# Performance work log

Measured on AMD Instinct MI355X. Metric: run time of the kernel, lower is better.

The kernel has to match this reference:

```python
import jax, jax.numpy as jnp
import numpy as np

N_HEAD = 16
HEAD_DIM = 64
N_EMBD = N_HEAD * HEAD_DIM  # 1024


def setup_inputs() -> dict:
    key = jax.random.key(0)
    ks = jax.random.split(key, 5)
    B, S = 2, 2048
    x = jax.random.normal(ks[0], (B, S, N_EMBD), dtype=jnp.float32)
    qkv_w = jax.random.normal(ks[1], (N_EMBD, 3 * N_EMBD), dtype=jnp.float32) * 0.02
    qkv_b = jax.random.normal(ks[2], (3 * N_EMBD,), dtype=jnp.float32) * 0.02
    proj_w = jax.random.normal(ks[3], (N_EMBD, N_EMBD), dtype=jnp.float32) * 0.02
    proj_b = jax.random.normal(ks[4], (N_EMBD,), dtype=jnp.float32) * 0.02
    return {"x": x, "qkv_w": qkv_w, "qkv_b": qkv_b, "proj_w": proj_w, "proj_b": proj_b}


def reference(x, qkv_w, qkv_b, proj_w, proj_b):
    B, S, _ = x.shape
    qkv = x @ qkv_w + qkv_b  # [B,S,3E]
    q, k, v = jnp.split(qkv, 3, axis=-1)
    # [B,H,S,D]
    q = q.reshape(B, S, N_HEAD, HEAD_DIM).transpose(0, 2, 1, 3)
    k = k.reshape(B, S, N_HEAD, HEAD_DIM).transpose(0, 2, 1, 3)
    v = v.reshape(B, S, N_HEAD, HEAD_DIM).transpose(0, 2, 1, 3)
    scale = 1.0 / jnp.sqrt(jnp.float32(HEAD_DIM))
    scores = jnp.einsum('bhqd,bhkd->bhqk', q, k) * scale  # [B,H,S,S]
    causal = jnp.tril(jnp.ones((S, S), dtype=bool))
    scores = jnp.where(causal[None, None], scores, jnp.float32(-jnp.inf))
    attn = jax.nn.softmax(scores, axis=-1)  # dropout p=0 (eval)
    out = jnp.einsum('bhqk,bhkd->bhqd', attn, v)
    out = out.transpose(0, 2, 1, 3).reshape(B, S, N_EMBD)
    out = out @ proj_w + proj_b  # resid dropout p=0
    return out, k, v
```

## Files before the change

### kernel.cpp

```cpp
#include <hip/hip_runtime.h>
#include <hip/hip_bf16.h>


typedef __attribute__((ext_vector_type(4))) float f32x4;
typedef __attribute__((ext_vector_type(16))) float f32x16;
typedef __attribute__((ext_vector_type(8))) short s16x8;
typedef __attribute__((ext_vector_type(4))) short s16x4;

__device__ __forceinline__ short f2bf(float f) {
    union { float f; unsigned u; } x{f};
    unsigned r = x.u + 0x7fff + ((x.u >> 16) & 1);
    return (short)(r >> 16);
}

__device__ __forceinline__ void gload_lds16(const void* g, void* l) {
    __builtin_amdgcn_global_load_lds(
        (const __attribute__((address_space(1))) void*)g,
        (__attribute__((address_space(3))) void*)l, 16, 0, 0);
}

__global__ __launch_bounds__(256) void fused_prepass(const float* __restrict__ x,
                                                     short* __restrict__ x_bf,
                                                     const float* __restrict__ qkv_w,
                                                     short* __restrict__ wT1,
                                                     const float* __restrict__ proj_w,
                                                     short* __restrict__ wT2) {
    __shared__ float tile[32][33];
    const int bid = blockIdx.x, tid = threadIdx.x;
    if (bid < 2048) {
        int i = (bid * 256 + tid) * 8;
        f32x4 a = *(const f32x4*)&x[i];
        f32x4 b = *(const f32x4*)&x[i + 4];
        s16x8 o;
        #pragma unroll
        for (int j = 0; j < 4; ++j) o[j] = f2bf(a[j]);
        #pragma unroll
        for (int j = 0; j < 4; ++j) o[j + 4] = f2bf(b[j]);
        *(s16x8*)&x_bf[i] = o;
        return;
    }
    const float* in;
    short* out;
    int K = 1024, N, n0, k0;
    if (bid < 5120) {
        int blk = bid - 2048;
        in = qkv_w; out = wT1; N = 3072;
        n0 = (blk % 96) * 32; k0 = (blk / 96) * 32;
    } else {
        int blk = bid - 5120;
        in = proj_w; out = wT2; N = 1024;
        n0 = (blk & 31) * 32; k0 = (blk >> 5) * 32;
    }
    const int tx = tid & 31, ty = tid >> 5;
    #pragma unroll
    for (int r = 0; r < 4; ++r)
        tile[ty + r * 8][tx] = in[(long)(k0 + ty + r * 8) * N + n0 + tx];
    __syncthreads();
    #pragma unroll
    for (int r = 0; r < 4; ++r)
        out[(long)(n0 + ty + r * 8) * K + k0 + tx] = f2bf(tile[tx][ty + r * 8]);
}

template <int MODE>
__global__ __launch_bounds__(256) void gemm_bf16(
    const short* __restrict__ A, const short* __restrict__ Bt,
    const float* __restrict__ bias, int M, int N, int K,
    float* __restrict__ outf,
    short* __restrict__ qbf, short* __restrict__ kbf, short* __restrict__ vbfT,
    float* __restrict__ kout, float* __restrict__ vout) {
    __shared__ __align__(16) short As[128 * 64];
    __shared__ __align__(16) short Bs[128 * 64];
    const int tid = threadIdx.x;
    const int l = tid & 63, w = tid >> 6;
    const int lr = l >> 4, lc = l & 15;
    const int wm = w >> 1, wn = w & 1;
    const int bid = blockIdx.x;
    const int xcd = bid & 7, s = bid >> 3;
    int bx, by;
    if (MODE == 1) { bx = (xcd & 1) * 12 + s % 12; by = (xcd >> 1) * 8 + s / 12; }
    else           { bx = (xcd & 1) * 4 + (s & 3); by = (xcd >> 1) * 8 + (s >> 2); }
    const int m0 = by * 128, n0 = bx * 128;

    f32x4 acc[4][4] = {};

    for (int kb = 0; kb < K; kb += 64) {
        __syncthreads();
        #pragma unroll
        for (int j = 0; j < 4; ++j) {
            const int c = tid + 256 * j;
            const int row = c >> 3;
            const int lseg = (c & 7) ^ (row & 7);
            gload_lds16(A + (long)(m0 + row) * K + kb + lseg * 8, As + c * 8);
            gload_lds16(Bt + (long)(n0 + row) * K + kb + lseg * 8, Bs + c * 8);
        }
        __syncthreads();
        #pragma unroll
        for (int kh = 0; kh < 2; ++kh) {
            s16x8 af[4], bfr[4];
            #pragma unroll
            for (int mi = 0; mi < 4; ++mi) {
                const int row = wm * 64 + mi * 16 + lc;
                af[mi] = *(const s16x8*)&As[row * 64 + (((kh * 4 + lr) ^ (lc & 7)) * 8)];
            }
            #pragma unroll
            for (int ni = 0; ni < 4; ++ni) {
                const int row = wn * 64 + ni * 16 + lc;
                bfr[ni] = *(const s16x8*)&Bs[row * 64 + (((kh * 4 + lr) ^ (lc & 7)) * 8)];
            }
            #pragma unroll
            for (int mi = 0; mi < 4; ++mi)
                #pragma unroll
                for (int ni = 0; ni < 4; ++ni)
                    acc[mi][ni] = __builtin_amdgcn_mfma_f32_16x16x32_bf16(
                        af[mi], bfr[ni], acc[mi][ni], 0, 0, 0);
        }
    }

    #pragma unroll
    for (int mi = 0; mi < 4; ++mi) {
        #pragma unroll
        for (int ni = 0; ni < 4; ++ni) {
            int col = n0 + wn * 64 + ni * 16 + lc;
            float bv = bias[col];
            if (MODE == 1) {
                int sec = col >> 10, rem = col & 1023;
                int h = rem >> 6, d = rem & 63;
                int row0 = m0 + wm * 64 + mi * 16 + lr * 4;
                int b = row0 >> 11, s0 = row0 & 2047;
                long idxSD = ((long)((b << 4) + h) * 2048 + s0) * 64 + d;
                if (sec == 0) {
                    #pragma unroll
                    for (int i = 0; i < 4; ++i) {
                        float val = acc[mi][ni][i] + bv;
                        qbf[idxSD + (long)i * 64] = f2bf(val * 0.1803368801111244f);
                    }
                } else if (sec == 1) {
                    #pragma unroll
                    for (int i = 0; i < 4; ++i) {
                        float val = acc[mi][ni][i] + bv;
                        kout[idxSD + (long)i * 64] = val;
                        kbf[idxSD + (long)i * 64] = f2bf(val);
                    }
                } else {
                    s16x4 pk;
                    #pragma unroll
                    for (int i = 0; i < 4; ++i) {
                        float val = acc[mi][ni][i] + bv;
                        vout[idxSD + (long)i * 64] = val;
                        pk[i] = f2bf(val);
                    }
                    *(s16x4*)&vbfT[((long)((b << 4) + h) * 64 + d) * 2048 + s0] = pk;
                }
            } else {
                #pragma unroll
                for (int i = 0; i < 4; ++i) {
                    int row = m0 + wm * 64 + mi * 16 + lr * 4 + i;
                    outf[(long)row * N + col] = acc[mi][ni][i] + bv;
                }
            }
        }
    }
}

__global__ __launch_bounds__(512, 4) void attn_kernel(const short* __restrict__ qbf,
                                                      const short* __restrict__ kbf,
                                                      const short* __restrict__ vbfT,
                                                      short* __restrict__ obf) {
    const int bid = blockIdx.x;
    const int xcd = bid & 7, r = bid >> 3;
    const int head_local = r & 3, q16 = r >> 2;
    const int qt = (q16 < 8) ? (q16 + 8) : (15 - q16);
    const int bh = xcd * 4 + head_local;
    const int tid = threadIdx.x;
    const int wv = tid >> 6, l = tid & 63;
    const int strip = wv & 3, kh = wv >> 2;
    const int h = l >> 5;
    const int l8 = l & 7;
    const int q0 = qt * 128 + strip * 32;
    const int qlane = q0 + (l & 31);
    const long baseSD = (long)bh * 2048 * 64;
    const long baseDS = (long)bh * 64 * 2048;

    __shared__ __align__(16) short Ks[2][64 * 64];
    __shared__ __align__(16) short Vs[2][64 * 64];
    __shared__ __align__(16) float MG[4][64][36];

    const int sSub = l >> 3;
    const int sChunk = (l & 7) ^ sSub;
    auto stage = [&](int kt, int nb) {
        const int k0 = kt * 64;
        const int r0 = wv * 8 + sSub;
        gload_lds16(kbf + baseSD + (long)(k0 + r0) * 64 + sChunk * 8,
                    &Ks[nb][(wv * 8) * 64]);
        gload_lds16(vbfT + baseDS + (long)r0 * 2048 + k0 + sChunk * 8,
                    &Vs[nb][(wv * 8) * 64]);
    };

    s16x8 qf[4];
    #pragma unroll
    for (int dd = 0; dd < 4; ++dd)
        qf[dd] = *(const s16x8*)&qbf[baseSD + (long)qlane * 64 + dd * 16 + h * 8];

    f32x4 lacc = {};
    f32x16 O[2] = {};

    const int nkt = 2 * qt + 2;

    stage(0, 0);
    __syncthreads();
    int cur = 0;

    for (int kt = 0; kt < nkt; ++kt) {
        if (kt + 1 < nkt) stage(kt + 1, cur ^ 1);
        const int kbase = kt * 64 + kh * 32;

        if (kbase <= q0 + 31) {
            const short* Kb = Ks[cur];
            const short* Vb = Vs[cur];
            f32x16 z = {};
            #pragma unroll
            for (int dd = 0; dd < 4; ++dd) {
                s16x8 kf = *(const s16x8*)&Kb[(kh * 32 + (l & 31)) * 64 +
                                              (((2 * dd + h) ^ l8) * 8)];
                z = __builtin_amdgcn_mfma_f32_32x32x16_bf16(kf, qf[dd], z, 0, 0, 0);
            }
            if (kbase + 31 > q0) {
                #pragma unroll
                for (int rr = 0; rr < 16; ++rr) {
                    int kpos = kbase + (rr & 3) + 8 * (rr >> 2) + 4 * h;
                    if (kpos > qlane) z[rr] = -INFINITY;
                }
            }
            float p[16];
            #pragma unroll
            for (int rr = 0; rr < 16; ++rr) {
                p[rr] = __builtin_amdgcn_exp2f(z[rr]);
                lacc[rr & 3] += p[rr];
            }
            #pragma unroll
            for (int f = 0; f < 2; ++f) {
                union { __hip_bfloat162 b2[4]; s16x8 v; } pk;
                #pragma unroll
                for (int j = 0; j < 4; ++j)
                    pk.b2[j] = __float22bfloat162_rn(
                        make_float2(p[f * 8 + 2 * j], p[f * 8 + 2 * j + 1]));
                const int c0 = kh * 4 + f * 2;
                #pragma unroll
                for (int dt2 = 0; dt2 < 2; ++dt2) {
                    const short* vr = &Vb[(dt2 * 32 + (l & 31)) * 64];
                    s16x8 vf;
                    *(s16x4*)&vf = *(const s16x4*)&vr[(c0 ^ l8) * 8 + 4 * h];
                    *(((s16x4*)&vf) + 1) = *(const s16x4*)&vr[((c0 + 1) ^ l8) * 8 + 4 * h];
                    O[dt2] = __builtin_amdgcn_mfma_f32_32x32x16_bf16(vf, pk.v,
                                                                     O[dt2], 0, 0, 0);
                }
            }
        }
        __syncthreads();
        cur ^= 1;
    }

    float lsum = (lacc[0] + lacc[1]) + (lacc[2] + lacc[3]);
    if (kh == 1) {
        float* row = &MG[strip][l][0];
        #pragma unroll
        for (int dt2 = 0; dt2 < 2; ++dt2)
            #pragma unroll
            for (int rr = 0; rr < 16; ++rr)
                row[dt2 * 16 + rr] = O[dt2][rr];
        row[32] = lsum;
    }
    __syncthreads();
    if (kh == 0) {
        const float* row = &MG[strip][l][0];
        lsum += row[32];
        lsum += __shfl_xor(lsum, 32);
        const int b = bh >> 4, hd = bh & 15;
        float inv = 1.0f / lsum;
        #pragma unroll
        for (int dt2 = 0; dt2 < 2; ++dt2) {
            #pragma unroll
            for (int g = 0; g < 4; ++g) {
                s16x4 o;
                #pragma unroll
                for (int i = 0; i < 4; ++i)
                    o[i] = f2bf((O[dt2][g * 4 + i] + row[dt2 * 16 + g * 4 + i]) * inv);
                const int d = dt2 * 32 + 8 * g + 4 * h;
                *(s16x4*)&obf[(long)(b * 2048 + qlane) * 1024 + hd * 64 + d] = o;
            }
        }
    }
}


extern "C" void kernel_launch(void* const* d_in, const int* in_sizes, int n_in,
                              void* d_out, int out_size, void* d_ws, size_t ws_size,
                              hipStream_t stream) {
    const float* x = (const float*)d_in[0];
    const float* qkv_w = (const float*)d_in[1];
    const float* qkv_b = (const float*)d_in[2];
    const float* proj_w = (const float*)d_in[3];
    const float* proj_b = (const float*)d_in[4];

    float* out = (float*)d_out;
    float* kout = out + 4194304;
    float* vout = out + 8388608;

    short* x_bf = (short*)d_ws;
    short* wT1 = x_bf + 4194304;
    short* wT2 = wT1 + 3145728;
    short* q_bf = wT2 + 1048576;
    short* k_bf = q_bf + 4194304;
    short* vT_bf = k_bf + 4194304;
    short* o_bf = x_bf;

    fused_prepass<<<6144, 256, 0, stream>>>(x, x_bf, qkv_w, wT1, proj_w, wT2);

    gemm_bf16<1><<<768, 256, 0, stream>>>(x_bf, wT1, qkv_b, 4096, 3072, 1024,
                                          nullptr, q_bf, k_bf, vT_bf, kout, vout);

    attn_kernel<<<512, 512, 0, stream>>>(q_bf, k_bf, vT_bf, o_bf);

    gemm_bf16<2><<<256, 256, 0, stream>>>(o_bf, wT2, proj_b, 4096, 1024, 1024,
                                          out, nullptr, nullptr, nullptr, nullptr, nullptr);
}
```

Baseline: 104.5 us.

## Split GEMM K dimension across two wave groups with LDS reduction

The GEMM block grows to 512 threads, split into two groups of four waves. Each group handles half of K (512) using its own LDS buffers. Group 1 then writes its partial accumulators to shared memory, and group 0 adds them before running the epilogue. The goal is more waves in flight per tile to hide load latency, especially for the proj GEMM, which has only 256 blocks. The costs are an extra LDS reduction pass, a hardcoded K=1024, and possible register-pressure issues under launch_bounds(512,4).

```diff
diff --git a/kernel.cpp b/kernel.cpp
--- a/kernel.cpp
+++ b/kernel.cpp
@@ -62,16 +62,17 @@
 }
 
 template <int MODE>
-__global__ __launch_bounds__(256) void gemm_bf16(
+__global__ __launch_bounds__(512, 4) void gemm_bf16(
     const short* __restrict__ A, const short* __restrict__ Bt,
     const float* __restrict__ bias, int M, int N, int K,
     float* __restrict__ outf,
     short* __restrict__ qbf, short* __restrict__ kbf, short* __restrict__ vbfT,
     float* __restrict__ kout, float* __restrict__ vout) {
-    __shared__ __align__(16) short As[128 * 64];
-    __shared__ __align__(16) short Bs[128 * 64];
+    __shared__ __align__(16) short As[2][128 * 64];
+    __shared__ __align__(16) short Bs[2][128 * 64];
     const int tid = threadIdx.x;
-    const int l = tid & 63, w = tid >> 6;
+    const int l = tid & 63, wv = tid >> 6;
+    const int grp = wv >> 2, w = wv & 3;
     const int lr = l >> 4, lc = l & 15;
     const int wm = w >> 1, wn = w & 1;
     const int bid = blockIdx.x;
@@ -80,18 +81,20 @@
     if (MODE == 1) { bx = (xcd & 1) * 12 + s % 12; by = (xcd >> 1) * 8 + s / 12; }
     else           { bx = (xcd & 1) * 4 + (s & 3); by = (xcd >> 1) * 8 + (s >> 2); }
     const int m0 = by * 128, n0 = bx * 128;
+    const int gtid = tid & 255;
 
     f32x4 acc[4][4] = {};
 
-    for (int kb = 0; kb < K; kb += 64) {
+    for (int it = 0; it < 8; ++it) {
+        const int kb = grp * 512 + it * 64;
         __syncthreads();
         #pragma unroll
         for (int j = 0; j < 4; ++j) {
-            const int c = tid + 256 * j;
+            const int c = gtid + 256 * j;
             const int row = c >> 3;
             const int lseg = (c & 7) ^ (row & 7);
-            gload_lds16(A + (long)(m0 + row) * K + kb + lseg * 8, As + c * 8);
-            gload_lds16(Bt + (long)(n0 + row) * K + kb + lseg * 8, Bs + c * 8);
+            gload_lds16(A + (long)(m0 + row) * K + kb + lseg * 8, &As[grp][c * 8]);
+            gload_lds16(Bt + (long)(n0 + row) * K + kb + lseg * 8, &Bs[grp][c * 8]);
         }
         __syncthreads();
         #pragma unroll
@@ -100,12 +103,12 @@
             #pragma unroll
             for (int mi = 0; mi < 4; ++mi) {
                 const int row = wm * 64 + mi * 16 + lc;
-                af[mi] = *(const s16x8*)&As[row * 64 + (((kh * 4 + lr) ^ (lc & 7)) * 8)];
+                af[mi] = *(const s16x8*)&As[grp][row * 64 + (((kh * 4 + lr) ^ (lc & 7)) * 8)];
             }
             #pragma unroll
             for (int ni = 0; ni < 4; ++ni) {
                 const int row = wn * 64 + ni * 16 + lc;
-                bfr[ni] = *(const s16x8*)&Bs[row * 64 + (((kh * 4 + lr) ^ (lc & 7)) * 8)];
+                bfr[ni] = *(const s16x8*)&Bs[grp][row * 64 + (((kh * 4 + lr) ^ (lc & 7)) * 8)];
             }
             #pragma unroll
             for (int mi = 0; mi < 4; ++mi)
@@ -115,6 +118,29 @@
                         af[mi], bfr[ni], acc[mi][ni], 0, 0, 0);
         }
     }
+
+    __syncthreads();
+    float* MB = (float*)&As[0][0];
+    float* reg = (w < 2) ? (float*)&As[w][0] : (float*)&Bs[w - 2][0];
+    if (grp == 1) {
+        #pragma unroll
+        for (int mi = 0; mi < 4; ++mi)
+            #pragma unroll
+            for (int ni = 0; ni < 4; ++ni)
+                #pragma unroll
+                for (int i = 0; i < 4; ++i)
+                    reg[(mi * 16 + lr * 4 + i) * 64 + ni * 16 + lc] = acc[mi][ni][i];
+    }
+    __syncthreads();
+    if (grp == 1) return;
+    #pragma unroll
+    for (int mi = 0; mi < 4; ++mi)
+        #pragma unroll
+        for (int ni = 0; ni < 4; ++ni)
+            #pragma unroll
+            for (int i = 0; i < 4; ++i)
+                acc[mi][ni][i] += reg[(mi * 16 + lr * 4 + i) * 64 + ni * 16 + lc];
+    (void)MB;
 
     #pragma unroll
     for (int mi = 0; mi < 4; ++mi) {
@@ -316,11 +342,11 @@
 
     fused_prepass<<<6144, 256, 0, stream>>>(x, x_bf, qkv_w, wT1, proj_w, wT2);
 
-    gemm_bf16<1><<<768, 256, 0, stream>>>(x_bf, wT1, qkv_b, 4096, 3072, 1024,
+    gemm_bf16<1><<<768, 512, 0, stream>>>(x_bf, wT1, qkv_b, 4096, 3072, 1024,
                                           nullptr, q_bf, k_bf, vT_bf, kout, vout);
 
     attn_kernel<<<512, 512, 0, stream>>>(q_bf, k_bf, vT_bf, o_bf);
 
-    gemm_bf16<2><<<256, 256, 0, stream>>>(o_bf, wT2, proj_b, 4096, 1024, 1024,
+    gemm_bf16<2><<<256, 512, 0, stream>>>(o_bf, wT2, proj_b, 4096, 1024, 1024,
                                           out, nullptr, nullptr, nullptr, nullptr, nullptr);
 }
```

Measured after the change: 111.0 us. 6.3% more time.
